# Kernel tuning notes

Measured on AMD Instinct MI355X. Metric: run time of the kernel, lower is better.

The kernel has to match this reference:

```python
import jax, jax.numpy as jnp
import numpy as np

N_PROTS = 2048
MOLS_PER_PROT = 8
N_MOLS = N_PROTS * MOLS_PER_PROT
DIM = 768
MARGIN = 0.5


def setup_inputs() -> dict:
    key = jax.random.key(0)
    k1, k2, k3 = jax.random.split(key, 3)
    prot_emb = jax.random.normal(k1, (N_PROTS, DIM), dtype=jnp.float32)
    mol_emb = jax.random.normal(k2, (N_MOLS, DIM), dtype=jnp.float32)
    # L2-normalize like typical CLIP-style retrieval embeddings
    prot_emb = prot_emb / jnp.linalg.norm(prot_emb, axis=1, keepdims=True)
    mol_emb = mol_emb / jnp.linalg.norm(mol_emb, axis=1, keepdims=True)
    # block-structured labels: protein i paired with mols [8i, 8i+8)
    rows = jnp.repeat(jnp.arange(N_PROTS), MOLS_PER_PROT)
    cols = jnp.arange(N_MOLS)
    labels = jnp.zeros((N_PROTS, N_MOLS), dtype=jnp.float32).at[rows, cols].set(1.0)
    # pIC50 values in [2, 10]
    pic50_matrix = 2.0 + 8.0 * jax.random.uniform(k3, (N_PROTS, N_MOLS), dtype=jnp.float32)
    logit_scale = jnp.float32(1.0 / 0.07)
    return {"prot_emb": prot_emb, "mol_emb": mol_emb, "labels": labels,
            "pic50_matrix": pic50_matrix, "logit_scale": logit_scale}


def reference(prot_emb, mol_emb, labels, pic50_matrix, logit_scale):
    n_prots = prot_emb.shape[0]
    n_mols = mol_emb.shape[0]
    sim = jnp.matmul(prot_emb, mol_emb.T) * logit_scale  # [n_prots, n_mols]

    # affinity-weighted InfoNCE (prot -> mol)
    pic50_norm = jnp.clip((pic50_matrix - 2.0) / 8.0, 0.0, 1.0)
    pos_w = labels * pic50_norm
    pos_w = pos_w / (pos_w.sum(axis=1, keepdims=True) + 1e-8)
    loss_p2m = -jnp.sum(pos_w * jax.nn.log_softmax(sim, axis=1)) / n_prots

    # mol -> prot NLL
    mol_labels = jnp.argmax(labels, axis=0)  # [n_mols]
    lsm_m2p = jax.nn.log_softmax(sim.T, axis=1)  # [n_mols, n_prots]
    loss_m2p = -jnp.mean(lsm_m2p[jnp.arange(n_mols), mol_labels])

    # pairwise margin-ranking among positives (exactly MOLS_PER_PROT positives per protein)
    P = MOLS_PER_PROT
    _, pos_idx = jax.lax.top_k(labels, P)  # [n_prots, P] indices of positives
    pos_pic = jnp.take_along_axis(pic50_matrix, pos_idx, axis=1)  # [n_prots, P]
    pos_sc = jnp.take_along_axis(sim, pos_idx, axis=1)            # [n_prots, P]
    dp = pos_pic[:, :, None] - pos_pic[:, None, :]  # [n_prots, P, P]
    ds = pos_sc[:, :, None] - pos_sc[:, None, :]
    pair = jnp.where(dp > 0, jax.nn.relu(MARGIN - ds),
                     jnp.where(dp < 0, jax.nn.relu(MARGIN + ds), 0.0))
    upper = jnp.triu(jnp.ones((P, P), dtype=bool), k=1)  # unordered pairs j<k
    n_pairs = n_prots * (P * (P - 1) // 2)
    ranking_loss = jnp.sum(jnp.where(upper[None], pair, 0.0)) / n_pairs

    # negative push-down
    neg_loss = jnp.mean(jax.nn.relu(sim * (1.0 - labels)))

    total = loss_p2m + loss_m2p + 0.5 * ranking_loss + 0.1 * neg_loss
    return (total, loss_p2m, loss_m2p, ranking_loss, neg_loss)
```

## Files before the change

### kernel.cpp

```cpp
#include <hip/hip_runtime.h>
#include <hip/hip_bf16.h>
#include <math.h>

#define N_PROTS 2048
#define N_MOLS  16384
#define DIM     768
#define SHIFT   16.0f
#define MARGIN  0.5f

typedef __attribute__((ext_vector_type(8))) short short8;
typedef __attribute__((ext_vector_type(4))) float f32x4;
typedef __attribute__((ext_vector_type(4))) unsigned short us4;
typedef __attribute__((ext_vector_type(8))) unsigned short us8;

__device__ __forceinline__ unsigned short bf16rnd(float x) {
    unsigned int u = __float_as_uint(x);
    u += 0x7fffu + ((u >> 16) & 1u);
    return (unsigned short)(u >> 16);
}

__device__ __forceinline__ void gload16(const void* g, void* l) {
    __builtin_amdgcn_global_load_lds(
        (const __attribute__((address_space(1))) unsigned int*)g,
        (__attribute__((address_space(3))) unsigned int*)l, 16, 0, 0);
}

#define ACC_FLOATS 34824
#define PROT_BF_OFF_B 139296ull
#define PROT_BF_BYTES (2048ull*768*2)
#define MOL_BF_OFF_B  (PROT_BF_OFF_B + PROT_BF_BYTES)
#define MOL_BF_BYTES  (16384ull*768*2)
#define WS_NEED       (MOL_BF_OFF_B + MOL_BF_BYTES)

__global__ __launch_bounds__(256)
void convert_bf16(const float* __restrict__ prot, const float* __restrict__ mol,
                  unsigned short* __restrict__ protBf, unsigned short* __restrict__ molBf)
{
    const size_t PROT_G = (size_t)N_PROTS * DIM / 8;
    size_t t = (size_t)blockIdx.x * 256 + threadIdx.x;
    const float* src;
    unsigned short* dst;
    if (t < PROT_G) { src = prot + t * 8; dst = protBf + t * 8; }
    else            { size_t u = t - PROT_G; src = mol + u * 8; dst = molBf + u * 8; }
    float4 v0 = ((const float4*)src)[0];
    float4 v1 = ((const float4*)src)[1];
    us8 o;
    o[0] = bf16rnd(v0.x); o[1] = bf16rnd(v0.y); o[2] = bf16rnd(v0.z); o[3] = bf16rnd(v0.w);
    o[4] = bf16rnd(v1.x); o[5] = bf16rnd(v1.y); o[6] = bf16rnd(v1.z); o[7] = bf16rnd(v1.w);
    *(us8*)dst = o;
}

__device__ __forceinline__ void epilogue(
    f32x4 acc[4][4], float scale, int rowBase, int colBase,
    int wave, int lane, int wr, int wc, int l15, int q,
    float* __restrict__ row_se, float* __restrict__ col_se,
    float* __restrict__ pos_sim, float* __restrict__ scalars, float* redBuf)
{
    float rsum[4][4];
    float csum[4] = {0.f, 0.f, 0.f, 0.f};
    float rl = 0.f;
#pragma unroll
    for (int mi = 0; mi < 4; ++mi)
#pragma unroll
        for (int r = 0; r < 4; ++r) rsum[mi][r] = 0.f;

#pragma unroll
    for (int mi = 0; mi < 4; ++mi) {
#pragma unroll
        for (int ni = 0; ni < 4; ++ni) {
#pragma unroll
            for (int r = 0; r < 4; ++r) {
                float sim = acc[mi][ni][r] * scale;
                float e = __expf(sim - SHIFT);
                rsum[mi][r] += e;
                csum[ni] += e;
                rl += fmaxf(sim, 0.f);
                int rg = rowBase + wr + mi * 16 + q * 4 + r;
                int cg = colBase + wc + ni * 16 + l15;
                if ((cg >> 3) == rg) pos_sim[cg] = sim;
            }
        }
    }

#pragma unroll
    for (int mi = 0; mi < 4; ++mi) {
#pragma unroll
        for (int r = 0; r < 4; ++r) {
            float v = rsum[mi][r];
            v += __shfl_xor(v, 1); v += __shfl_xor(v, 2);
            v += __shfl_xor(v, 4); v += __shfl_xor(v, 8);
            if (l15 == 0)
                atomicAdd(&row_se[rowBase + wr + mi * 16 + q * 4 + r], v);
        }
    }
#pragma unroll
    for (int ni = 0; ni < 4; ++ni) {
        float v = csum[ni];
        v += __shfl_xor(v, 16); v += __shfl_xor(v, 32);
        if (q == 0)
            atomicAdd(&col_se[colBase + wc + ni * 16 + l15], v);
    }
#pragma unroll
    for (int m = 1; m < 64; m <<= 1) rl += __shfl_xor(rl, m);
    if (lane == 0) redBuf[wave] = rl;
    __syncthreads();
    if (wave == 0 && lane == 0)
        atomicAdd(&scalars[0], redBuf[0] + redBuf[1] + redBuf[2] + redBuf[3]);
}

__global__ __launch_bounds__(256, 4)
void sim_pass_bf16(const unsigned short* __restrict__ protBf,
                   const unsigned short* __restrict__ molBf,
                   const float* __restrict__ scale_p,
                   float* __restrict__ row_se, float* __restrict__ col_se,
                   float* __restrict__ pos_sim, float* __restrict__ scalars)
{
    __shared__ unsigned short As[2][128][32];
    __shared__ unsigned short Bs[2][128][32];
    __shared__ float redBuf[4];

    const int tid = threadIdx.x;
    const int rowBase = blockIdx.y * 128;
    const int colBase = blockIdx.x * 128;
    const int wave = tid >> 6;
    const int lane = tid & 63;
    const int wr = (wave >> 1) * 64;
    const int wc = (wave & 1) * 64;
    const int l15 = lane & 15;
    const int q   = lane >> 4;

    f32x4 acc[4][4];
#pragma unroll
    for (int i = 0; i < 4; ++i)
#pragma unroll
        for (int j = 0; j < 4; ++j) acc[i][j] = (f32x4){0.f, 0.f, 0.f, 0.f};

    const int r0   = tid >> 2;
    const int csrc = ((tid & 3) ^ ((r0 >> 1) & 3)) << 3;
    const unsigned short* aP0 = protBf + (size_t)(rowBase + r0) * DIM + csrc;
    const unsigned short* aP1 = aP0 + (size_t)64 * DIM;
    const unsigned short* bP0 = molBf + (size_t)(colBase + r0) * DIM + csrc;
    const unsigned short* bP1 = bP0 + (size_t)64 * DIM;
    unsigned short* ldsA0 = &As[0][0][0] + (wave << 9);
    unsigned short* ldsB0 = &Bs[0][0][0] + (wave << 9);

    gload16(aP0, ldsA0);
    gload16(aP1, ldsA0 + 2048);
    gload16(bP0, ldsB0);
    gload16(bP1, ldsB0 + 2048);

#pragma unroll 1
    for (int s = 0; s < DIM / 32; ++s) {
        const int cur = s & 1;
        __syncthreads();

        if (s + 1 < DIM / 32) {
            const int ko = (s + 1) * 32;
            const int nb = (cur ^ 1) * 4096;
            gload16(aP0 + ko, ldsA0 + nb);
            gload16(aP1 + ko, ldsA0 + nb + 2048);
            gload16(bP0 + ko, ldsB0 + nb);
            gload16(bP1 + ko, ldsB0 + nb + 2048);
        }

        short8 aF[4], bF[4];
#pragma unroll
        for (int mi = 0; mi < 4; ++mi) {
            const int R = wr + mi * 16 + l15;
            aF[mi] = *(const short8*)&As[cur][R][(q ^ ((R >> 1) & 3)) << 3];
        }
#pragma unroll
        for (int ni = 0; ni < 4; ++ni) {
            const int R = wc + ni * 16 + l15;
            bF[ni] = *(const short8*)&Bs[cur][R][(q ^ ((R >> 1) & 3)) << 3];
        }
#pragma unroll
        for (int mi = 0; mi < 4; ++mi)
#pragma unroll
            for (int ni = 0; ni < 4; ++ni)
                acc[mi][ni] = __builtin_amdgcn_mfma_f32_16x16x32_bf16(aF[mi], bF[ni], acc[mi][ni], 0, 0, 0);
    }

    epilogue(acc, scale_p[0], rowBase, colBase, wave, lane, wr, wc, l15, q,
             row_se, col_se, pos_sim, scalars, redBuf);
}

__global__ __launch_bounds__(256, 2)
void sim_pass(const float* __restrict__ prot, const float* __restrict__ mol,
              const float* __restrict__ scale_p,
              float* __restrict__ row_se, float* __restrict__ col_se,
              float* __restrict__ pos_sim, float* __restrict__ scalars)
{
    __shared__ unsigned short As[128][32];
    __shared__ unsigned short Bs[128][32];
    __shared__ float redBuf[4];

    const int tid = threadIdx.x;
    const int rowBase = blockIdx.y * 128;
    const int colBase = blockIdx.x * 128;
    const int wave = tid >> 6;
    const int lane = tid & 63;
    const int wr = (wave >> 1) * 64;
    const int wc = (wave & 1) * 64;
    const int l15 = lane & 15;
    const int q   = lane >> 4;

    f32x4 acc[4][4];
#pragma unroll
    for (int i = 0; i < 4; ++i)
#pragma unroll
        for (int j = 0; j < 4; ++j) acc[i][j] = (f32x4){0.f, 0.f, 0.f, 0.f};

    const float* aBase = prot + (size_t)rowBase * DIM;
    const float* bBase = mol  + (size_t)colBase * DIM;
    float4 aReg[4], bReg[4];
#pragma unroll
    for (int i = 0; i < 4; ++i) {
        int f = tid + 256 * i;
        int row = f >> 3, c4 = f & 7;
        aReg[i] = *(const float4*)(aBase + (size_t)row * DIM + (c4 << 2));
        bReg[i] = *(const float4*)(bBase + (size_t)row * DIM + (c4 << 2));
    }
#pragma unroll 1
    for (int s = 0; s < DIM / 32; ++s) {
#pragma unroll
        for (int i = 0; i < 4; ++i) {
            int f = tid + 256 * i;
            int row = f >> 3, c4 = f & 7;
            us4 av, bv;
            av.x = bf16rnd(aReg[i].x); av.y = bf16rnd(aReg[i].y);
            av.z = bf16rnd(aReg[i].z); av.w = bf16rnd(aReg[i].w);
            bv.x = bf16rnd(bReg[i].x); bv.y = bf16rnd(bReg[i].y);
            bv.z = bf16rnd(bReg[i].z); bv.w = bf16rnd(bReg[i].w);
            *(us4*)&As[row][c4 << 2] = av;
            *(us4*)&Bs[row][c4 << 2] = bv;
        }
        __syncthreads();
        if (s + 1 < DIM / 32) {
            int k0 = (s + 1) * 32;
#pragma unroll
            for (int i = 0; i < 4; ++i) {
                int f = tid + 256 * i;
                int row = f >> 3, c4 = f & 7;
                aReg[i] = *(const float4*)(aBase + (size_t)row * DIM + k0 + (c4 << 2));
                bReg[i] = *(const float4*)(bBase + (size_t)row * DIM + k0 + (c4 << 2));
            }
        }
        short8 aF[4], bF[4];
#pragma unroll
        for (int mi = 0; mi < 4; ++mi) aF[mi] = *(const short8*)&As[wr + mi * 16 + l15][q * 8];
#pragma unroll
        for (int ni = 0; ni < 4; ++ni) bF[ni] = *(const short8*)&Bs[wc + ni * 16 + l15][q * 8];
#pragma unroll
        for (int mi = 0; mi < 4; ++mi)
#pragma unroll
            for (int ni = 0; ni < 4; ++ni)
                acc[mi][ni] = __builtin_amdgcn_mfma_f32_16x16x32_bf16(aF[mi], bF[ni], acc[mi][ni], 0, 0, 0);
        __syncthreads();
    }

    epilogue(acc, scale_p[0], rowBase, colBase, wave, lane, wr, wc, l15, q,
             row_se, col_se, pos_sim, scalars, redBuf);
}

__global__ __launch_bounds__(256)
void finalize1(const float* __restrict__ row_se, const float* __restrict__ col_se,
               const float* __restrict__ pos_sim, const float* __restrict__ pic50,
               float* __restrict__ scalars)
{
    int j = blockIdx.x * 256 + threadIdx.x;
    float m2p = SHIFT + __logf(col_se[j]) - pos_sim[j];

    float p2m = 0.f, rank = 0.f, prelu = 0.f;
    if ((j & 7) == 0) {
        int i = j >> 3;
        float s[8], pc[8], pr[8];
#pragma unroll
        for (int p = 0; p < 8; ++p) {
            s[p]  = pos_sim[j + p];
            pr[p] = pic50[(size_t)i * N_MOLS + j + p];
            float x = (pr[p] - 2.0f) * 0.125f;
            pc[p] = fminf(fmaxf(x, 0.f), 1.f);
            prelu += fmaxf(s[p], 0.f);
        }
        float wsum = 1e-8f;
#pragma unroll
        for (int p = 0; p < 8; ++p) wsum += pc[p];
        float lse = SHIFT + __logf(row_se[i]);
        float accp = 0.f;
#pragma unroll
        for (int p = 0; p < 8; ++p) accp += pc[p] * (lse - s[p]);
        p2m = accp / wsum;
#pragma unroll
        for (int a = 0; a < 8; ++a)
#pragma unroll
            for (int b = a + 1; b < 8; ++b) {
                float dp = pr[a] - pr[b];
                float ds = s[a] - s[b];
                float v = (dp > 0.f) ? fmaxf(MARGIN - ds, 0.f)
                        : ((dp < 0.f) ? fmaxf(MARGIN + ds, 0.f) : 0.f);
                rank += v;
            }
    }

#pragma unroll
    for (int m = 1; m < 64; m <<= 1) {
        m2p   += __shfl_xor(m2p, m);
        p2m   += __shfl_xor(p2m, m);
        rank  += __shfl_xor(rank, m);
        prelu += __shfl_xor(prelu, m);
    }
    __shared__ float rbuf[4][4];
    int wave = threadIdx.x >> 6, lane = threadIdx.x & 63;
    if (lane == 0) { rbuf[wave][0] = m2p; rbuf[wave][1] = p2m; rbuf[wave][2] = rank; rbuf[wave][3] = prelu; }
    __syncthreads();
    if (threadIdx.x == 0) {
        float a = 0, b = 0, c = 0, d = 0;
        for (int w = 0; w < 4; ++w) { a += rbuf[w][0]; b += rbuf[w][1]; c += rbuf[w][2]; d += rbuf[w][3]; }
        atomicAdd(&scalars[2], a);
        atomicAdd(&scalars[1], b);
        atomicAdd(&scalars[3], c);
        atomicAdd(&scalars[4], d);
    }
}

__global__ void finalize2(const float* __restrict__ scalars, float* __restrict__ out)
{
    float relu_neg = scalars[0] - scalars[4];
    float p2m  = scalars[1] / (float)N_PROTS;
    float m2p  = scalars[2] / (float)N_MOLS;
    float rank = scalars[3] / ((float)N_PROTS * 28.0f);
    float neg  = relu_neg / ((float)N_PROTS * (float)N_MOLS);
    out[0] = p2m + m2p + 0.5f * rank + 0.1f * neg;
    out[1] = p2m;
    out[2] = m2p;
    out[3] = rank;
    out[4] = neg;
}

extern "C" void kernel_launch(void* const* d_in, const int* in_sizes, int n_in,
                              void* d_out, int out_size, void* d_ws, size_t ws_size,
                              hipStream_t stream) {
    const float* prot   = (const float*)d_in[0];
    const float* mol    = (const float*)d_in[1];
    const float* pic50  = (const float*)d_in[3];
    const float* lscale = (const float*)d_in[4];

    float* ws      = (float*)d_ws;
    float* row_se  = ws;
    float* col_se  = ws + 2048;
    float* pos_sim = ws + 2048 + 16384;
    float* scalars = ws + 2048 + 16384 + 16384;

    hipMemsetAsync(d_ws, 0, (size_t)ACC_FLOATS * sizeof(float), stream);

    dim3 grid(N_MOLS / 128, N_PROTS / 128);
    if (ws_size >= WS_NEED) {
        unsigned short* protBf = (unsigned short*)((char*)d_ws + PROT_BF_OFF_B);
        unsigned short* molBf  = (unsigned short*)((char*)d_ws + MOL_BF_OFF_B);
        size_t groups = ((size_t)N_PROTS + N_MOLS) * DIM / 8;
        convert_bf16<<<(unsigned)(groups / 256), 256, 0, stream>>>(prot, mol, protBf, molBf);
        sim_pass_bf16<<<grid, 256, 0, stream>>>(protBf, molBf, lscale, row_se, col_se, pos_sim, scalars);
    } else {
        sim_pass<<<grid, 256, 0, stream>>>(prot, mol, lscale, row_se, col_se, pos_sim, scalars);
    }
    finalize1<<<N_MOLS / 256, 256, 0, stream>>>(row_se, col_se, pos_sim, pic50, scalars);
    finalize2<<<1, 1, 0, stream>>>(scalars, (float*)d_out);
}
```

Baseline: 400.6 us.

## Enlarge bf16 GEMM tile to 256x256 with XCD-aware block remapping

The bf16 similarity kernel now computes 256x256 output tiles with 512 threads (8 waves, each 64x128), where it previously used 128x128 tiles. Blocks are remapped so that consecutive block ids on the same XCD share column panels for L2 reuse. Larger tiles cut global/LDS loads per FLOP and the number of atomics per element. In exchange, each wave now holds 128 fp32 accumulator registers, and the grid has only 512 blocks, which may hurt occupancy and load balance on the device's CUs. The epilogue helper is inlined into both kernels.

```diff
diff --git a/kernel.cpp b/kernel.cpp
--- a/kernel.cpp
+++ b/kernel.cpp
@@ -50,24 +50,100 @@
     *(us8*)dst = o;
 }
 
-__device__ __forceinline__ void epilogue(
-    f32x4 acc[4][4], float scale, int rowBase, int colBase,
-    int wave, int lane, int wr, int wc, int l15, int q,
-    float* __restrict__ row_se, float* __restrict__ col_se,
-    float* __restrict__ pos_sim, float* __restrict__ scalars, float* redBuf)
+__global__ __launch_bounds__(512, 4)
+void sim_pass_bf16(const unsigned short* __restrict__ protBf,
+                   const unsigned short* __restrict__ molBf,
+                   const float* __restrict__ scale_p,
+                   float* __restrict__ row_se, float* __restrict__ col_se,
+                   float* __restrict__ pos_sim, float* __restrict__ scalars)
 {
+    __shared__ unsigned short As[2][256][32];
+    __shared__ unsigned short Bs[2][256][32];
+    __shared__ float redBuf[8];
+
+    const int tid = threadIdx.x;
+    const int l    = blockIdx.y * 64 + blockIdx.x;
+    const int xcd  = l & 7;
+    const int slot = l >> 3;
+    const int bx   = xcd * 8 + (slot & 7);
+    const int by   = slot >> 3;
+    const int rowBase = by * 256;
+    const int colBase = bx * 256;
+
+    const int wave = tid >> 6;
+    const int lane = tid & 63;
+    const int wr = (wave >> 1) * 64;
+    const int wc = (wave & 1) * 128;
+    const int l15 = lane & 15;
+    const int q   = lane >> 4;
+
+    f32x4 acc[4][8];
+#pragma unroll
+    for (int i = 0; i < 4; ++i)
+#pragma unroll
+        for (int j = 0; j < 8; ++j) acc[i][j] = (f32x4){0.f, 0.f, 0.f, 0.f};
+
+    const int r0   = tid >> 2;
+    const int csrc = ((tid & 3) ^ ((r0 >> 1) & 3)) << 3;
+    const unsigned short* aP0 = protBf + (size_t)(rowBase + r0) * DIM + csrc;
+    const unsigned short* aP1 = aP0 + (size_t)128 * DIM;
+    const unsigned short* bP0 = molBf + (size_t)(colBase + r0) * DIM + csrc;
+    const unsigned short* bP1 = bP0 + (size_t)128 * DIM;
+    unsigned short* ldsA0 = &As[0][0][0] + (wave << 9);
+    unsigned short* ldsB0 = &Bs[0][0][0] + (wave << 9);
+
+    gload16(aP0, ldsA0);
+    gload16(aP1, ldsA0 + 4096);
+    gload16(bP0, ldsB0);
+    gload16(bP1, ldsB0 + 4096);
+
+#pragma unroll 1
+    for (int s = 0; s < DIM / 32; ++s) {
+        const int cur = s & 1;
+        __syncthreads();
+
+        if (s + 1 < DIM / 32) {
+            const int ko = (s + 1) * 32;
+            const int nb = (cur ^ 1) * 8192;
+            gload16(aP0 + ko, ldsA0 + nb);
+            gload16(aP1 + ko, ldsA0 + nb + 4096);
+            gload16(bP0 + ko, ldsB0 + nb);
+            gload16(bP1 + ko, ldsB0 + nb + 4096);
+        }
+
+        short8 aF[4], bF[8];
+#pragma unroll
+        for (int mi = 0; mi < 4; ++mi) {
+            const int R = wr + mi * 16 + l15;
+            aF[mi] = *(const short8*)&As[cur][R][(q ^ ((R >> 1) & 3)) << 3];
+        }
+#pragma unroll
+        for (int ni = 0; ni < 8; ++ni) {
+            const int R = wc + ni * 16 + l15;
+            bF[ni] = *(const short8*)&Bs[cur][R][(q ^ ((R >> 1) & 3)) << 3];
+        }
+#pragma unroll
+        for (int mi = 0; mi < 4; ++mi)
+#pragma unroll
+            for (int ni = 0; ni < 8; ++ni)
+                acc[mi][ni] = __builtin_amdgcn_mfma_f32_16x16x32_bf16(aF[mi], bF[ni], acc[mi][ni], 0, 0, 0);
+    }
+
+    const float scale = scale_p[0];
     float rsum[4][4];
-    float csum[4] = {0.f, 0.f, 0.f, 0.f};
+    float csum[8];
     float rl = 0.f;
 #pragma unroll
     for (int mi = 0; mi < 4; ++mi)
 #pragma unroll
         for (int r = 0; r < 4; ++r) rsum[mi][r] = 0.f;
+#pragma unroll
+    for (int ni = 0; ni < 8; ++ni) csum[ni] = 0.f;
 
 #pragma unroll
     for (int mi = 0; mi < 4; ++mi) {
 #pragma unroll
-        for (int ni = 0; ni < 4; ++ni) {
+        for (int ni = 0; ni < 8; ++ni) {
 #pragma unroll
             for (int r = 0; r < 4; ++r) {
                 float sim = acc[mi][ni][r] * scale;
@@ -94,7 +170,7 @@
         }
     }
 #pragma unroll
-    for (int ni = 0; ni < 4; ++ni) {
+    for (int ni = 0; ni < 8; ++ni) {
         float v = csum[ni];
         v += __shfl_xor(v, 16); v += __shfl_xor(v, 32);
         if (q == 0)
@@ -104,85 +180,11 @@
     for (int m = 1; m < 64; m <<= 1) rl += __shfl_xor(rl, m);
     if (lane == 0) redBuf[wave] = rl;
     __syncthreads();
-    if (wave == 0 && lane == 0)
-        atomicAdd(&scalars[0], redBuf[0] + redBuf[1] + redBuf[2] + redBuf[3]);
-}
-
-__global__ __launch_bounds__(256, 4)
-void sim_pass_bf16(const unsigned short* __restrict__ protBf,
-                   const unsigned short* __restrict__ molBf,
-                   const float* __restrict__ scale_p,
-                   float* __restrict__ row_se, float* __restrict__ col_se,
-                   float* __restrict__ pos_sim, float* __restrict__ scalars)
-{
-    __shared__ unsigned short As[2][128][32];
-    __shared__ unsigned short Bs[2][128][32];
-    __shared__ float redBuf[4];
-
-    const int tid = threadIdx.x;
-    const int rowBase = blockIdx.y * 128;
-    const int colBase = blockIdx.x * 128;
-    const int wave = tid >> 6;
-    const int lane = tid & 63;
-    const int wr = (wave >> 1) * 64;
-    const int wc = (wave & 1) * 64;
-    const int l15 = lane & 15;
-    const int q   = lane >> 4;
-
-    f32x4 acc[4][4];
-#pragma unroll
-    for (int i = 0; i < 4; ++i)
-#pragma unroll
-        for (int j = 0; j < 4; ++j) acc[i][j] = (f32x4){0.f, 0.f, 0.f, 0.f};
-
-    const int r0   = tid >> 2;
-    const int csrc = ((tid & 3) ^ ((r0 >> 1) & 3)) << 3;
-    const unsigned short* aP0 = protBf + (size_t)(rowBase + r0) * DIM + csrc;
-    const unsigned short* aP1 = aP0 + (size_t)64 * DIM;
-    const unsigned short* bP0 = molBf + (size_t)(colBase + r0) * DIM + csrc;
-    const unsigned short* bP1 = bP0 + (size_t)64 * DIM;
-    unsigned short* ldsA0 = &As[0][0][0] + (wave << 9);
-    unsigned short* ldsB0 = &Bs[0][0][0] + (wave << 9);
-
-    gload16(aP0, ldsA0);
-    gload16(aP1, ldsA0 + 2048);
-    gload16(bP0, ldsB0);
-    gload16(bP1, ldsB0 + 2048);
-
-#pragma unroll 1
-    for (int s = 0; s < DIM / 32; ++s) {
-        const int cur = s & 1;
-        __syncthreads();
-
-        if (s + 1 < DIM / 32) {
-            const int ko = (s + 1) * 32;
-            const int nb = (cur ^ 1) * 4096;
-            gload16(aP0 + ko, ldsA0 + nb);
-            gload16(aP1 + ko, ldsA0 + nb + 2048);
-            gload16(bP0 + ko, ldsB0 + nb);
-            gload16(bP1 + ko, ldsB0 + nb + 2048);
-        }
-
-        short8 aF[4], bF[4];
-#pragma unroll
-        for (int mi = 0; mi < 4; ++mi) {
-            const int R = wr + mi * 16 + l15;
-            aF[mi] = *(const short8*)&As[cur][R][(q ^ ((R >> 1) & 3)) << 3];
-        }
-#pragma unroll
-        for (int ni = 0; ni < 4; ++ni) {
-            const int R = wc + ni * 16 + l15;
-            bF[ni] = *(const short8*)&Bs[cur][R][(q ^ ((R >> 1) & 3)) << 3];
-        }
-#pragma unroll
-        for (int mi = 0; mi < 4; ++mi)
-#pragma unroll
-            for (int ni = 0; ni < 4; ++ni)
-                acc[mi][ni] = __builtin_amdgcn_mfma_f32_16x16x32_bf16(aF[mi], bF[ni], acc[mi][ni], 0, 0, 0);
-    }
-
-    epilogue(acc, scale_p[0], rowBase, colBase, wave, lane, wr, wc, l15, q,
-             row_se, col_se, pos_sim, scalars, redBuf);
+    if (tid == 0) {
+        float t = 0.f;
+        for (int w = 0; w < 8; ++w) t += redBuf[w];
+        atomicAdd(&scalars[0], t);
+    }
 }
 
 __global__ __launch_bounds__(256, 2)
@@ -259,8 +261,55 @@
         __syncthreads();
     }
 
-    epilogue(acc, scale_p[0], rowBase, colBase, wave, lane, wr, wc, l15, q,
-             row_se, col_se, pos_sim, scalars, redBuf);
+    const float scale = scale_p[0];
+    float rsum[4][4];
+    float csum[4] = {0.f, 0.f, 0.f, 0.f};
+    float rl = 0.f;
+#pragma unroll
+    for (int mi = 0; mi < 4; ++mi)
+#pragma unroll
+        for (int r = 0; r < 4; ++r) rsum[mi][r] = 0.f;
+#pragma unroll
+    for (int mi = 0; mi < 4; ++mi) {
+#pragma unroll
+        for (int ni = 0; ni < 4; ++ni) {
+#pragma unroll
+            for (int r = 0; r < 4; ++r) {
+                float sim = acc[mi][ni][r] * scale;
+                float e = __expf(sim - SHIFT);
+                rsum[mi][r] += e;
+                csum[ni] += e;
+                rl += fmaxf(sim, 0.f);
+                int rg = rowBase + wr + mi * 16 + q * 4 + r;
+                int cg = colBase + wc + ni * 16 + l15;
+                if ((cg >> 3) == rg) pos_sim[cg] = sim;
+            }
+        }
+    }
+#pragma unroll
+    for (int mi = 0; mi < 4; ++mi) {
+#pragma unroll
+        for (int r = 0; r < 4; ++r) {
+            float v = rsum[mi][r];
+            v += __shfl_xor(v, 1); v += __shfl_xor(v, 2);
+            v += __shfl_xor(v, 4); v += __shfl_xor(v, 8);
+            if (l15 == 0)
+                atomicAdd(&row_se[rowBase + wr + mi * 16 + q * 4 + r], v);
+        }
+    }
+#pragma unroll
+    for (int ni = 0; ni < 4; ++ni) {
+        float v = csum[ni];
+        v += __shfl_xor(v, 16); v += __shfl_xor(v, 32);
+        if (q == 0)
+            atomicAdd(&col_se[colBase + wc + ni * 16 + l15], v);
+    }
+#pragma unroll
+    for (int m = 1; m < 64; m <<= 1) rl += __shfl_xor(rl, m);
+    if (lane == 0) redBuf[wave] = rl;
+    __syncthreads();
+    if (tid == 0)
+        atomicAdd(&scalars[0], redBuf[0] + redBuf[1] + redBuf[2] + redBuf[3]);
 }
 
 __global__ __launch_bounds__(256)
@@ -354,14 +403,15 @@
 
     hipMemsetAsync(d_ws, 0, (size_t)ACC_FLOATS * sizeof(float), stream);
 
-    dim3 grid(N_MOLS / 128, N_PROTS / 128);
     if (ws_size >= WS_NEED) {
         unsigned short* protBf = (unsigned short*)((char*)d_ws + PROT_BF_OFF_B);
         unsigned short* molBf  = (unsigned short*)((char*)d_ws + MOL_BF_OFF_B);
         size_t groups = ((size_t)N_PROTS + N_MOLS) * DIM / 8;
         convert_bf16<<<(unsigned)(groups / 256), 256, 0, stream>>>(prot, mol, protBf, molBf);
-        sim_pass_bf16<<<grid, 256, 0, stream>>>(protBf, molBf, lscale, row_se, col_se, pos_sim, scalars);
+        dim3 grid(64, 8);
+        sim_pass_bf16<<<grid, 512, 0, stream>>>(protBf, molBf, lscale, row_se, col_se, pos_sim, scalars);
     } else {
+        dim3 grid(N_MOLS / 128, N_PROTS / 128);
         sim_pass<<<grid, 256, 0, stream>>>(prot, mol, lscale, row_se, col_se, pos_sim, scalars);
     }
     finalize1<<<N_MOLS / 256, 256, 0, stream>>>(row_se, col_se, pos_sim, pic50, scalars);
```

Result: slower. 686.0 us (+71.2%).
